# Performance work log

Hardware: AMD Instinct MI355X
Metric: run time of the kernel (lower is better)

The kernel has to match this reference:

```python
import jax, jax.numpy as jnp
import numpy as np
import math

D_MODEL = 1024
N_HEADS = 16
RANK = 16
SCALE = 16.0
T_LEN = 2048
BSZ = 2


def setup_inputs() -> dict:
    key = jax.random.key(0)
    ks = jax.random.split(key, 12)
    d, r = D_MODEL, RANK
    inp = {
        "query": jax.random.normal(ks[0], (T_LEN, BSZ, d), dtype=jnp.float32),
        "key": jax.random.normal(ks[1], (T_LEN, BSZ, d), dtype=jnp.float32),
        "value": jax.random.normal(ks[2], (T_LEN, BSZ, d), dtype=jnp.float32),
        "need_weights": 0,
        "attn_mask": 0,
        "in_proj_weight": jax.random.normal(ks[3], (3 * d, d), dtype=jnp.float32) * 0.02,
        "in_proj_bias": jax.random.normal(ks[4], (3 * d,), dtype=jnp.float32) * 0.02,
        "out_w": jax.random.normal(ks[5], (d, d), dtype=jnp.float32) * 0.02,
        "out_b": jax.random.normal(ks[6], (d,), dtype=jnp.float32) * 0.02,
        "k_a": jax.random.normal(ks[7], (r, d), dtype=jnp.float32) * 0.02,
        "k_b": jax.random.normal(ks[8], (r, d), dtype=jnp.float32) * 0.02,
        "v_a": jax.random.normal(ks[9], (r, d), dtype=jnp.float32) * 0.02,
        "v_b": jax.random.normal(ks[10], (r, d), dtype=jnp.float32) * 0.02,
    }
    return inp


def reference(query, key, value, need_weights, attn_mask,
              in_proj_weight, in_proj_bias, out_w, out_b,
              k_a, k_b, v_a, v_b):
    # NOTE: original module computes q,k,v all from `query` (self-attention);
    # `key`, `value`, `need_weights`, `attn_mask` are unused in the math.
    T, B, d = query.shape
    H = N_HEADS
    hd = d // H
    qkv = query @ in_proj_weight.T + in_proj_bias  # (T, B, 3d)
    q, k, v = jnp.split(qkv, 3, axis=-1)
    s = SCALE / RANK
    # LoRA low-rank updates on K and V (computed from query)
    k = k + s * ((query @ k_a.T) @ k_b)
    v = v + s * ((query @ v_a.T) @ v_b)
    # split heads: (T, B, H, hd)
    qh = q.reshape(T, B, H, hd)
    kh = k.reshape(T, B, H, hd)
    vh = v.reshape(T, B, H, hd)
    scale = 1.0 / math.sqrt(hd)
    scores = jnp.einsum('tbhd,sbhd->bhts', qh * scale, kh)  # (B, H, T, T)
    attn = jax.nn.softmax(scores, axis=-1)
    out = jnp.einsum('bhts,sbhd->tbhd', attn, vh).reshape(T, B, d)
    out = out @ out_w.T + out_b
    return out
```

## Files before the change

### kernel.cpp

```cpp
#include <hip/hip_runtime.h>
#include <stdint.h>

#define DEVI __device__ __forceinline__

typedef unsigned short u16;
typedef __attribute__((ext_vector_type(4))) float f32x4;
typedef __attribute__((ext_vector_type(16))) float f32x16;
typedef __attribute__((ext_vector_type(8))) short bf16x8;
typedef __attribute__((ext_vector_type(2))) unsigned int u32x2;

constexpr int T_LEN = 2048;
constexpr int BSZ   = 2;
constexpr int DM    = 1024;
constexpr int NH    = 16;
constexpr int HD    = 64;
constexpr int MROWS = T_LEN * BSZ;
constexpr float LORA_S = 16.0f / 16.0f;
constexpr float QSCALE = 0.125f * 1.4426950408889634f;

DEVI u16 f2bf(float x) {
  union { float f; uint32_t u; } v; v.f = x;
  uint32_t r = (v.u + 0x7FFFu + ((v.u >> 16) & 1u)) >> 16;
  return (u16)r;
}

DEVI uint32_t pk2bf(float a, float b) {
  return (uint32_t)f2bf(a) | ((uint32_t)f2bf(b) << 16);
}

DEVI uint32_t e2r(float x) {
  union { float f; uint32_t u; } v;
  v.f = __builtin_amdgcn_exp2f(x);
  return v.u + 0x8000u;
}

DEVI void gload_lds16(const void* g, void* l) {
  __builtin_amdgcn_global_load_lds(
      (const __attribute__((address_space(1))) void*)g,
      (__attribute__((address_space(3))) void*)l, 16, 0, 0);
}

DEVI f32x4 mfma16(bf16x8 a, bf16x8 b, f32x4 c) {
  return __builtin_amdgcn_mfma_f32_16x16x32_bf16(a, b, c, 0, 0, 0);
}
DEVI f32x16 mfma32(bf16x8 a, bf16x8 b, f32x16 c) {
  return __builtin_amdgcn_mfma_f32_32x32x16_bf16(a, b, c, 0, 0, 0);
}

DEVI int swz16(int row, int c8) { return row * 64 + ((c8 ^ (row & 7)) << 3); }

DEVI int kvswz(int rc, int l) { return rc * 128 + ((l ^ (rc & 15)) << 3); }

__global__ void prep_kernel(const float* __restrict__ query,
                            const float* __restrict__ W,
                            const float* __restrict__ ka, const float* __restrict__ kb,
                            const float* __restrict__ va, const float* __restrict__ vb,
                            const float* __restrict__ ow,
                            u16* __restrict__ Wm, u16* __restrict__ Wo,
                            u16* __restrict__ Aq) {
  const int W3 = 3 * DM * DM;
  const int WO = DM * DM;
  const int AQ = MROWS * DM;
  const int total = W3 + WO + AQ;
  for (int idx = blockIdx.x * blockDim.x + threadIdx.x; idx < total;
       idx += gridDim.x * blockDim.x) {
    if (idx < W3) {
      const int n = idx >> 10, k = idx & 1023;
      float w = W[idx];
      if (n >= 2 * DM) {
        const int n2 = n - 2 * DM;
        float a = 0.f;
#pragma unroll
        for (int r = 0; r < 16; ++r) a += va[r * DM + k] * vb[r * DM + n2];
        w += LORA_S * a;
      } else if (n >= DM) {
        const int n2 = n - DM;
        float a = 0.f;
#pragma unroll
        for (int r = 0; r < 16; ++r) a += ka[r * DM + k] * kb[r * DM + n2];
        w += LORA_S * a;
      }
      Wm[idx] = f2bf(w);
    } else if (idx < W3 + WO) {
      const int i = idx - W3;
      Wo[i] = f2bf(ow[i]);
    } else {
      const int i = idx - W3 - WO;
      Aq[i] = f2bf(query[i]);
    }
  }
}

template <int EPIL>
__global__ __launch_bounds__(256) void gemm_bt(
    const u16* __restrict__ A, const u16* __restrict__ Bt,
    const float* __restrict__ bias, float* __restrict__ Cf,
    u16* __restrict__ Qb, u16* __restrict__ Kb, u16* __restrict__ Vt,
    int M, int N, int K) {
  constexpr int BM = 128, BN = 128, BK = 64;
  __shared__ alignas(16) u16 SM[2][(BM + BN) * BK];
  const int tid = threadIdx.x;
  const int wv = tid >> 6, ln = tid & 63;
  const int l16 = ln & 15, lhi = ln >> 4;
  const int row0 = blockIdx.x * BM, col0 = blockIdx.y * BN;
  const int wr = (wv >> 1) * 64, wc = (wv & 1) * 64;

  f32x4 acc[4][4];
#pragma unroll
  for (int i = 0; i < 4; ++i)
#pragma unroll
    for (int j = 0; j < 4; ++j) acc[i][j] = f32x4{0.f, 0.f, 0.f, 0.f};

  const int srow = ln >> 3;
  const int scol = (((ln & 7) ^ (ln >> 3)) & 7) * 8;

  auto stage = [&](int buf, int ks) {
    const int k0 = ks * BK;
    u16* Al = SM[buf];
    u16* Bl = SM[buf] + BM * BK;
#pragma unroll
    for (int it = 0; it < 4; ++it) {
      const int c = wv * 4 + it;
      gload_lds16(A + (size_t)(row0 + c * 8 + srow) * K + k0 + scol, &Al[c * 512]);
      gload_lds16(Bt + (size_t)(col0 + c * 8 + srow) * K + k0 + scol, &Bl[c * 512]);
    }
  };

  const int NS = K / BK;
  stage(0, 0);
  __syncthreads();
  int cur = 0;
  for (int t = 0; t < NS; ++t) {
    if (t + 1 < NS) stage(cur ^ 1, t + 1);
    const u16* Al = SM[cur];
    const u16* Bl = SM[cur] + BM * BK;
#pragma unroll
    for (int ks = 0; ks < 2; ++ks) {
      bf16x8 af[4], bfr[4];
#pragma unroll
      for (int m = 0; m < 4; ++m)
        af[m] = *(const bf16x8*)&Al[swz16(wr + m * 16 + l16, ks * 4 + lhi)];
#pragma unroll
      for (int n = 0; n < 4; ++n)
        bfr[n] = *(const bf16x8*)&Bl[swz16(wc + n * 16 + l16, ks * 4 + lhi)];
#pragma unroll
      for (int m = 0; m < 4; ++m)
#pragma unroll
        for (int n = 0; n < 4; ++n) acc[m][n] = mfma16(af[m], bfr[n], acc[m][n]);
    }
    __syncthreads();
    cur ^= 1;
  }

  if constexpr (EPIL == 0) {
    if (col0 >= 2 * DM) {
      u16* Cl = SM[0];
#pragma unroll
      for (int m = 0; m < 4; ++m)
#pragma unroll
        for (int n = 0; n < 4; ++n) {
          const int lc = wc + n * 16 + l16;
          const float bc = bias[col0 + lc];
#pragma unroll
          for (int r = 0; r < 4; ++r) {
            const int rl = wr + m * 16 + lhi * 4 + r;
            const int tl = rl >> 1, bb = rl & 1;
            Cl[lc * 128 + bb * 64 + (((tl >> 3) ^ (lc & 7)) << 3) + (tl & 7)] =
                f2bf(acc[m][n][r] + bc);
          }
        }
      __syncthreads();
      const int h0 = (col0 - 2 * DM) >> 6;
      const int t0 = row0 >> 1;
#pragma unroll
      for (int i = 0; i < 8; ++i) {
        const int cid = i * 256 + tid;
        const int lc = cid >> 4, bb = (cid >> 3) & 1, tc = cid & 7;
        bf16x8 ch = *(const bf16x8*)&Cl[lc * 128 + bb * 64 + ((tc ^ (lc & 7)) << 3)];
        const int h = h0 + (lc >> 6), dd = lc & 63;
        *(bf16x8*)&Vt[(((size_t)(bb * NH + h)) * HD + dd) * T_LEN + t0 + tc * 8] = ch;
      }
      return;
    }
  }

#pragma unroll
  for (int m = 0; m < 4; ++m) {
#pragma unroll
    for (int n = 0; n < 4; ++n) {
      const int col = col0 + wc + n * 16 + l16;
      const float bc = bias[col];
#pragma unroll
      for (int r = 0; r < 4; ++r) {
        const int row = row0 + wr + m * 16 + lhi * 4 + r;
        const float v = acc[m][n][r] + bc;
        if constexpr (EPIL == 0) {
          const int t = row >> 1, b = row & 1;
          if (col < DM) {
            const int h = col >> 6, dd = col & 63;
            Qb[(((size_t)(b * NH + h)) * T_LEN + t) * HD + dd] = f2bf(v * QSCALE);
          } else {
            const int c2 = col - DM, h = c2 >> 6, dd = c2 & 63;
            Kb[(((size_t)(b * NH + h)) * T_LEN + t) * HD + dd] = f2bf(v);
          }
        } else {
          Cf[(size_t)row * N + col] = v;
        }
      }
    }
  }
}

__global__ __launch_bounds__(256) void attn_kernel(const u16* __restrict__ Qb,
                                                   const u16* __restrict__ Kb,
                                                   const u16* __restrict__ Vt,
                                                   u16* __restrict__ Ob) {
  constexpr int KBLK = 64;
  constexpr int NT = T_LEN / KBLK;
  __shared__ alignas(16) u16 Kl[2][32 * 128];
  __shared__ alignas(16) u16 Vl[2][32 * 128];

  const int tid = threadIdx.x;
  const int wv = tid >> 6, ln = tid & 63;
  const int l32 = ln & 31, hi = ln >> 5;

  const int bid = blockIdx.x;
  const int lb = (bid & 7) * 64 + (bid >> 3);
  const int bh = lb >> 4;
  const int b = bh >> 4, h = bh & 15;
  const int q0 = (lb & 15) * 128 + wv * 32;

  const u16* Qh = Qb + (size_t)bh * T_LEN * HD;
  const u16* Kh = Kb + (size_t)bh * T_LEN * HD;
  const u16* Vh = Vt + (size_t)bh * HD * T_LEN;

  bf16x8 qf[4];
#pragma unroll
  for (int kd = 0; kd < 4; ++kd)
    qf[kd] = *(const bf16x8*)&Qh[(size_t)(q0 + l32) * HD + kd * 16 + hi * 8];

  bf16x8 ones;
#pragma unroll
  for (int i = 0; i < 8; ++i) ones[i] = (short)0x3F80;

  f32x16 ot[2] = {f32x16{}, f32x16{}};
  f32x16 lacc = f32x16{};

  const int g_row = ln >> 4;
  const int g_s   = ln & 15;

  auto stage = [&](int buf, int kt) {
    const int kt0 = kt * KBLK;
#pragma unroll
    for (int it = 0; it < 2; ++it) {
      const int j = wv * 2 + it;
      const int row = 4 * j + g_row;
      const int l = g_s ^ (row & 15);
      const int lr = row + 32 * (l >> 3);
      const int c8 = l & 7;
      gload_lds16(Kh + (size_t)(kt0 + lr) * HD + c8 * 8, &Kl[buf][j * 512]);
      gload_lds16(Vh + (size_t)lr * T_LEN + kt0 + c8 * 8, &Vl[buf][j * 512]);
    }
  };

  stage(0, 0);
  __syncthreads();
  int cur = 0;
  for (int kt = 0; kt < NT; ++kt) {
    if (kt + 1 < NT) stage(cur ^ 1, kt + 1);

    f32x16 st[2] = {f32x16{}, f32x16{}};
#pragma unroll
    for (int kd = 0; kd < 4; ++kd) {
      bf16x8 k0 = *(const bf16x8*)&Kl[cur][kvswz(l32, kd * 2 + hi)];
      bf16x8 k1 = *(const bf16x8*)&Kl[cur][kvswz(l32, 8 + kd * 2 + hi)];
      st[0] = mfma32(k0, qf[kd], st[0]);
      st[1] = mfma32(k1, qf[kd], st[1]);
    }

    uint32_t c[2][8];
#pragma unroll
    for (int mk = 0; mk < 2; ++mk)
#pragma unroll
      for (int d = 0; d < 8; ++d)
        c[mk][d] = __builtin_amdgcn_perm(e2r(st[mk][2 * d + 1]),
                                         e2r(st[mk][2 * d]), 0x07060302u);

#pragma unroll
    for (int ksl = 0; ksl < 4; ++ksl) {
      const int mk = ksl >> 1, s2 = ksl & 1;
      uint32_t a0 = c[mk][4 * s2 + 0], b0 = c[mk][4 * s2 + 2];
      uint32_t a1 = c[mk][4 * s2 + 1], b1 = c[mk][4 * s2 + 3];
      u32x2 r0 = __builtin_amdgcn_permlane32_swap(a0, b0, false, false);
      u32x2 r1 = __builtin_amdgcn_permlane32_swap(a1, b1, false, false);
      union { bf16x8 v; uint32_t u[4]; } pu;
      pu.u[0] = r0[0]; pu.u[1] = r1[0]; pu.u[2] = r0[1]; pu.u[3] = r1[1];
      bf16x8 vf0 = *(const bf16x8*)&Vl[cur][kvswz(l32, ksl * 2 + hi)];
      bf16x8 vf1 = *(const bf16x8*)&Vl[cur][kvswz(l32, 8 + ksl * 2 + hi)];
      ot[0] = mfma32(vf0, pu.v, ot[0]);
      ot[1] = mfma32(vf1, pu.v, ot[1]);
      lacc = mfma32(ones, pu.v, lacc);
    }
    __syncthreads();
    cur ^= 1;
  }

  const float inv = 1.0f / lacc[0];
  const size_t rowbase = ((size_t)(q0 + l32) * BSZ + b) * DM + h * HD;
#pragma unroll
  for (int dt = 0; dt < 2; ++dt) {
#pragma unroll
    for (int g = 0; g < 4; ++g) {
      const float v0 = ot[dt][4 * g + 0] * inv;
      const float v1 = ot[dt][4 * g + 1] * inv;
      const float v2 = ot[dt][4 * g + 2] * inv;
      const float v3 = ot[dt][4 * g + 3] * inv;
      u32x2 w; w[0] = pk2bf(v0, v1); w[1] = pk2bf(v2, v3);
      const int dim = dt * 32 + 8 * g + 4 * hi;
      *(u32x2*)&Ob[rowbase + dim] = w;
    }
  }
}

extern "C" void kernel_launch(void* const* d_in, const int* in_sizes, int n_in,
                              void* d_out, int out_size, void* d_ws, size_t ws_size,
                              hipStream_t stream) {
  const float* query = (const float*)d_in[0];
  const float* W     = (const float*)d_in[5];
  const float* bias  = (const float*)d_in[6];
  const float* ow    = (const float*)d_in[7];
  const float* ob    = (const float*)d_in[8];
  const float* ka    = (const float*)d_in[9];
  const float* kb    = (const float*)d_in[10];
  const float* va    = (const float*)d_in[11];
  const float* vb    = (const float*)d_in[12];

  char* ws = (char*)d_ws;
  u16* Wm = (u16*)ws; ws += (size_t)3 * DM * DM * 2;
  u16* Wo = (u16*)ws; ws += (size_t)DM * DM * 2;
  u16* Aq = (u16*)ws; ws += (size_t)MROWS * DM * 2;
  u16* Qb = (u16*)ws; ws += (size_t)BSZ * NH * T_LEN * HD * 2;
  u16* Kb = (u16*)ws; ws += (size_t)BSZ * NH * T_LEN * HD * 2;
  u16* Vt = (u16*)ws; ws += (size_t)BSZ * NH * T_LEN * HD * 2;
  u16* Ob = (u16*)ws; ws += (size_t)MROWS * DM * 2;

  prep_kernel<<<2048, 256, 0, stream>>>(query, W, ka, kb, va, vb, ow, Wm, Wo, Aq);

  gemm_bt<0><<<dim3(MROWS / 128, (3 * DM) / 128), 256, 0, stream>>>(
      Aq, Wm, bias, nullptr, Qb, Kb, Vt, MROWS, 3 * DM, DM);

  attn_kernel<<<512, 256, 0, stream>>>(Qb, Kb, Vt, Ob);

  gemm_bt<1><<<dim3(MROWS / 128, DM / 128), 256, 0, stream>>>(
      Ob, Wo, ob, (float*)d_out, nullptr, nullptr, nullptr, MROWS, DM, DM);
}
```

Before: 124.4 us.

## Deepen attention K/V pipeline to four LDS stages with explicit vmcnt barriers

Replaces the double-buffered K/V staging in the attention kernel with a 4-buffer ring that keeps three tiles of async global-to-LDS loads in flight. Each step waits with a partial vmcnt and a raw s_barrier instead of a full __syncthreads, and the source pointers are precomputed and incremented. The aim is to hide global load latency better. In exchange, LDS use per block doubles, which can reduce occupancy.

```diff
diff --git a/kernel.cpp b/kernel.cpp
--- a/kernel.cpp
+++ b/kernel.cpp
@@ -50,6 +50,14 @@
 DEVI int swz16(int row, int c8) { return row * 64 + ((c8 ^ (row & 7)) << 3); }
 
 DEVI int kvswz(int rc, int l) { return rc * 128 + ((l ^ (rc & 15)) << 3); }
+
+#define WAITBAR(N)                                        \
+  do {                                                    \
+    asm volatile("s_waitcnt vmcnt(" #N ")" ::: "memory"); \
+    __builtin_amdgcn_sched_barrier(0);                    \
+    __builtin_amdgcn_s_barrier();                         \
+    __builtin_amdgcn_sched_barrier(0);                    \
+  } while (0)
 
 __global__ void prep_kernel(const float* __restrict__ query,
                             const float* __restrict__ W,
@@ -217,8 +225,7 @@
                                                    u16* __restrict__ Ob) {
   constexpr int KBLK = 64;
   constexpr int NT = T_LEN / KBLK;
-  __shared__ alignas(16) u16 Kl[2][32 * 128];
-  __shared__ alignas(16) u16 Vl[2][32 * 128];
+  __shared__ alignas(16) u16 KV[4][2][32 * 128];
 
   const int tid = threadIdx.x;
   const int wv = tid >> 6, ln = tid & 63;
@@ -248,36 +255,36 @@
 
   const int g_row = ln >> 4;
   const int g_s   = ln & 15;
-
-  auto stage = [&](int buf, int kt) {
-    const int kt0 = kt * KBLK;
-#pragma unroll
-    for (int it = 0; it < 2; ++it) {
-      const int j = wv * 2 + it;
-      const int row = 4 * j + g_row;
-      const int l = g_s ^ (row & 15);
-      const int lr = row + 32 * (l >> 3);
-      const int c8 = l & 7;
-      gload_lds16(Kh + (size_t)(kt0 + lr) * HD + c8 * 8, &Kl[buf][j * 512]);
-      gload_lds16(Vh + (size_t)lr * T_LEN + kt0 + c8 * 8, &Vl[buf][j * 512]);
-    }
+  const int j0 = wv * 2, j1 = wv * 2 + 1;
+  const int row0r = 4 * j0 + g_row, row1r = 4 * j1 + g_row;
+  const int l0 = g_s ^ (row0r & 15), l1 = g_s ^ (row1r & 15);
+  const int lr0 = row0r + 32 * (l0 >> 3), lr1 = row1r + 32 * (l1 >> 3);
+  const int c80 = (l0 & 7) * 8, c81 = (l1 & 7) * 8;
+
+  const u16* ks0 = Kh + (size_t)lr0 * HD + c80;
+  const u16* ks1 = Kh + (size_t)lr1 * HD + c81;
+  const u16* vs0 = Vh + (size_t)lr0 * T_LEN + c80;
+  const u16* vs1 = Vh + (size_t)lr1 * T_LEN + c81;
+
+  auto stagep = [&](int buf) {
+    gload_lds16(ks0, &KV[buf][0][j0 * 512]);
+    gload_lds16(ks1, &KV[buf][0][j1 * 512]);
+    gload_lds16(vs0, &KV[buf][1][j0 * 512]);
+    gload_lds16(vs1, &KV[buf][1][j1 * 512]);
+    ks0 += KBLK * HD; ks1 += KBLK * HD; vs0 += KBLK; vs1 += KBLK;
   };
 
-  stage(0, 0);
-  __syncthreads();
-  int cur = 0;
-  for (int kt = 0; kt < NT; ++kt) {
-    if (kt + 1 < NT) stage(cur ^ 1, kt + 1);
-
+  auto compute = [&](int buf) {
+    const u16* Kl = KV[buf][0];
+    const u16* Vl = KV[buf][1];
     f32x16 st[2] = {f32x16{}, f32x16{}};
 #pragma unroll
     for (int kd = 0; kd < 4; ++kd) {
-      bf16x8 k0 = *(const bf16x8*)&Kl[cur][kvswz(l32, kd * 2 + hi)];
-      bf16x8 k1 = *(const bf16x8*)&Kl[cur][kvswz(l32, 8 + kd * 2 + hi)];
+      bf16x8 k0 = *(const bf16x8*)&Kl[kvswz(l32, kd * 2 + hi)];
+      bf16x8 k1 = *(const bf16x8*)&Kl[kvswz(l32, 8 + kd * 2 + hi)];
       st[0] = mfma32(k0, qf[kd], st[0]);
       st[1] = mfma32(k1, qf[kd], st[1]);
     }
-
     uint32_t c[2][8];
 #pragma unroll
     for (int mk = 0; mk < 2; ++mk)
@@ -285,7 +292,6 @@
       for (int d = 0; d < 8; ++d)
         c[mk][d] = __builtin_amdgcn_perm(e2r(st[mk][2 * d + 1]),
                                          e2r(st[mk][2 * d]), 0x07060302u);
-
 #pragma unroll
     for (int ksl = 0; ksl < 4; ++ksl) {
       const int mk = ksl >> 1, s2 = ksl & 1;
@@ -295,15 +301,26 @@
       u32x2 r1 = __builtin_amdgcn_permlane32_swap(a1, b1, false, false);
       union { bf16x8 v; uint32_t u[4]; } pu;
       pu.u[0] = r0[0]; pu.u[1] = r1[0]; pu.u[2] = r0[1]; pu.u[3] = r1[1];
-      bf16x8 vf0 = *(const bf16x8*)&Vl[cur][kvswz(l32, ksl * 2 + hi)];
-      bf16x8 vf1 = *(const bf16x8*)&Vl[cur][kvswz(l32, 8 + ksl * 2 + hi)];
+      bf16x8 vf0 = *(const bf16x8*)&Vl[kvswz(l32, ksl * 2 + hi)];
+      bf16x8 vf1 = *(const bf16x8*)&Vl[kvswz(l32, 8 + ksl * 2 + hi)];
       ot[0] = mfma32(vf0, pu.v, ot[0]);
       ot[1] = mfma32(vf1, pu.v, ot[1]);
       lacc = mfma32(ones, pu.v, lacc);
     }
-    __syncthreads();
-    cur ^= 1;
-  }
+  };
+
+  stagep(0); stagep(1); stagep(2);
+
+  for (int t4 = 0; t4 < NT - 4; t4 += 4) {
+    WAITBAR(8); compute(0); stagep(3);
+    WAITBAR(8); compute(1); stagep(0);
+    WAITBAR(8); compute(2); stagep(1);
+    WAITBAR(8); compute(3); stagep(2);
+  }
+  WAITBAR(8); compute(0); stagep(3);
+  WAITBAR(8); compute(1);
+  WAITBAR(4); compute(2);
+  WAITBAR(0); compute(3);
 
   const float inv = 1.0f / lacc[0];
   const size_t rowbase = ((size_t)(q0 + l32) * BSZ + b) * DM + h * HD;
```

New measurement: 115.4 us. 7.2% less time.
